# Kernel optimization log

Measured on AMD Instinct MI355X. Metric: run time of the kernel, lower is better.

The kernel has to match this reference:

```python
import jax, jax.numpy as jnp
import numpy as np

C_Z = 128
C_HIDDEN = 128
EPS = 1e-5


def _layer_norm(x, w, b):
    mu = jnp.mean(x, axis=-1, keepdims=True)
    var = jnp.var(x, axis=-1, keepdims=True)
    return (x - mu) * jax.lax.rsqrt(var + EPS) * w + b


def setup_inputs() -> dict:
    key = jax.random.key(0)
    ks = jax.random.split(key, 8)
    B, N = 1, 384
    z = jax.random.normal(ks[0], (B, N, N, C_Z), dtype=jnp.float32)
    mask = jnp.ones((B, N, N), dtype=jnp.float32)
    s_z = 1.0 / np.sqrt(C_Z)
    s_h = 1.0 / np.sqrt(C_HIDDEN)
    return {
        "z": z,
        "mask": mask,
        # projection linears (lecun-like random init)
        "w_ap": jax.random.normal(ks[1], (C_HIDDEN, C_Z), jnp.float32) * s_z,
        "b_ap": jnp.zeros((C_HIDDEN,), jnp.float32),
        "w_bp": jax.random.normal(ks[2], (C_HIDDEN, C_Z), jnp.float32) * s_z,
        "b_bp": jnp.zeros((C_HIDDEN,), jnp.float32),
        # gating linears: torch init is zeros weight / ones bias, but use small
        # random weights so gradients are non-trivial; bias = 1 as in 'gating' init
        "w_ag": jax.random.normal(ks[3], (C_HIDDEN, C_Z), jnp.float32) * s_z,
        "b_ag": jnp.ones((C_HIDDEN,), jnp.float32),
        "w_bg": jax.random.normal(ks[4], (C_HIDDEN, C_Z), jnp.float32) * s_z,
        "b_bg": jnp.ones((C_HIDDEN,), jnp.float32),
        "w_g": jax.random.normal(ks[5], (C_Z, C_Z), jnp.float32) * s_z,
        "b_g": jnp.ones((C_Z,), jnp.float32),
        # final output linear ('final' init is zeros; randomize for a useful baseline)
        "w_z": jax.random.normal(ks[6], (C_Z, C_HIDDEN), jnp.float32) * s_h,
        "b_z": jnp.zeros((C_Z,), jnp.float32),
        "ln_in_w": jnp.ones((C_Z,), jnp.float32),
        "ln_in_b": jnp.zeros((C_Z,), jnp.float32),
        "ln_out_w": jnp.ones((C_HIDDEN,), jnp.float32),
        "ln_out_b": jnp.zeros((C_HIDDEN,), jnp.float32),
    }


def reference(z, mask, w_ap, b_ap, w_bp, b_bp, w_ag, b_ag, w_bg, b_bg,
              w_g, b_g, w_z, b_z, ln_in_w, ln_in_b, ln_out_w, ln_out_b):
    # z: [B, N, N, C_z], mask: [B, N, N]
    m = mask[..., None]
    zn = _layer_norm(z, ln_in_w, ln_in_b)
    a = (zn @ w_ap.T + b_ap) * jax.nn.sigmoid(zn @ w_ag.T + b_ag) * m
    b = (zn @ w_bp.T + b_bp) * jax.nn.sigmoid(zn @ w_bg.T + b_bg) * m
    # outgoing: a -> [B,C,i,j], b -> [B,C,j,i]
    a_p = jnp.transpose(a, (0, 3, 1, 2))
    b_p = jnp.transpose(b, (0, 3, 2, 1))
    # NOTE: repo's einsum has no contracted index -> elementwise product a*b
    x = jnp.einsum('bcij,bcji->bijc', a_p, b_p)  # [B, N, N, C_hidden]
    x = _layer_norm(x, ln_out_w, ln_out_b)
    x = x @ w_z.T + b_z
    g = jax.nn.sigmoid(zn @ w_g.T + b_g)
    return x * g
```

## Files before the change

kernel.cpp:

```cpp
#include <hip/hip_runtime.h>

#define NN 384
#define CC 128
#define PP (NN*NN)
#define PB 64
#define NB (PP/PB)
#define TPB 256

typedef __attribute__((ext_vector_type(8))) short bf16x8;
typedef __attribute__((ext_vector_type(4))) float f32x4;
typedef __attribute__((ext_vector_type(8))) unsigned short u16x8;

#define PL_APH 0
#define PL_AGH 1
#define PL_BPH 2
#define PL_BGH 3
#define PL_APL 4
#define PL_AGL 5
#define PL_BPL 6
#define PL_BGL 7
#define PL_G   8
#define PL_Z   9

__device__ __forceinline__ unsigned short f2bf(float f){
  unsigned u = __float_as_uint(f);
  u += 0x7FFFu + ((u>>16)&1u);
  return (unsigned short)(u>>16);
}
__device__ __forceinline__ float bf2f(unsigned h){
  return __uint_as_float(h<<16);
}
__device__ __forceinline__ unsigned pack2(float a, float b){
  return (unsigned)f2bf(a) | ((unsigned)f2bf(b)<<16);
}
__device__ __forceinline__ float sigmoidf_(float x){
  return __fdividef(1.0f, 1.0f + __expf(-x));
}

__global__ __launch_bounds__(256) void k0_wprep(
    const float* __restrict__ wap, const float* __restrict__ wag,
    const float* __restrict__ wbp, const float* __restrict__ wbg,
    const float* __restrict__ wg,  const float* __restrict__ wz,
    unsigned short* __restrict__ wfrag){
  int tid = blockIdx.x*256 + threadIdx.x;
  int plane = tid >> 11;
  int chunk = tid & 2047;
  int mat = (plane < 8) ? (plane & 3) : (plane == 8 ? 4 : 5);
  bool lo = (plane >= 4) && (plane < 8);
  const float* W = (mat==0)?wap:(mat==1)?wag:(mat==2)?wbp:(mat==3)?wbg:(mat==4)?wg:wz;
  int k0 = chunk >> 9, n = (chunk >> 6) & 7, l = chunk & 63;
  int o  = n*16 + (l & 15);
  int kb = k0*32 + ((l>>4)<<3);
  const float* s = W + o*128 + kb;
  u16x8 v;
  #pragma unroll
  for (int e=0;e<8;e++){
    float w = s[e];
    unsigned short h = f2bf(w);
    v[e] = lo ? f2bf(w - bf2f(h)) : h;
  }
  *(u16x8*)(wfrag + (size_t)tid*8) = v;
}

__device__ __forceinline__ void stage_plane(const unsigned short* __restrict__ g,
                                            unsigned char* slot, int t){
  int wv = t>>6, l = t&63;
#if defined(__has_builtin) && __has_builtin(__builtin_amdgcn_global_load_lds)
  const unsigned char* src = (const unsigned char*)g + wv*8192 + l*16;
  unsigned char* dst = slot + wv*8192;
  #pragma unroll
  for (int i=0;i<8;i++)
    __builtin_amdgcn_global_load_lds(
        (const __attribute__((address_space(1))) unsigned int*)(src + i*1024),
        (__attribute__((address_space(3))) unsigned int*)(dst + i*1024),
        16, 0, 0);
#else
  #pragma unroll
  for (int i=0;i<8;i++)
    *(uint4*)(slot + i*4096 + t*16) =
        *(const uint4*)((const unsigned char*)g + i*4096 + t*16);
#endif
}

__device__ __forceinline__ void pass_HL(const bf16x8 aH[4], const bf16x8 aL[4],
    const unsigned char* w, int l, f32x4 acc[8]){
  #pragma unroll
  for (int k0=0;k0<4;k0++){
    #pragma unroll
    for (int n=0;n<8;n++){
      bf16x8 f = *(const bf16x8*)(w + ((k0*8+n)*64 + l)*16);
      acc[n] = __builtin_amdgcn_mfma_f32_16x16x32_bf16(aH[k0], f, acc[n], 0,0,0);
      acc[n] = __builtin_amdgcn_mfma_f32_16x16x32_bf16(aL[k0], f, acc[n], 0,0,0);
    }
  }
}

__device__ __forceinline__ void pass_H(const bf16x8 a[4],
    const unsigned char* w, int l, f32x4 acc[8]){
  #pragma unroll
  for (int k0=0;k0<4;k0++){
    #pragma unroll
    for (int n=0;n<8;n++){
      bf16x8 f = *(const bf16x8*)(w + ((k0*8+n)*64 + l)*16);
      acc[n] = __builtin_amdgcn_mfma_f32_16x16x32_bf16(a[k0], f, acc[n], 0,0,0);
    }
  }
}

__device__ __forceinline__ void bias_init(const float* __restrict__ b, int l, f32x4 acc[8]){
  #pragma unroll
  for (int n=0;n<8;n++){
    float v = b[n*16 + (l&15)];
    f32x4 iv = {v,v,v,v};
    acc[n]=iv;
  }
}

__global__ __launch_bounds__(TPB,2) void k_fused(
    const float* __restrict__ z, const float* __restrict__ mask,
    const float* __restrict__ bap, const float* __restrict__ bag,
    const float* __restrict__ bbp, const float* __restrict__ bbg,
    const float* __restrict__ bgg, const float* __restrict__ bz,
    const float* __restrict__ lniw, const float* __restrict__ lnib,
    const float* __restrict__ lnow, const float* __restrict__ lnob,
    const unsigned short* __restrict__ wfrag,
    float* __restrict__ out){
  __shared__ unsigned char lds[65536];
  unsigned char* bufH  = lds;
  unsigned char* bufL  = lds + 16384;
  unsigned char* wslot = lds + 32768;
  const int t = threadIdx.x;
  const int pos0 = blockIdx.x * PB;
  const int rowg = t>>5, c4 = (t&31)<<2;

  stage_plane(wfrag + PL_APH*16384, wslot, t);

  {
    float4 lw = *(const float4*)(lniw + c4);
    float4 lb = *(const float4*)(lnib + c4);
    #pragma unroll
    for (int it=0; it<8; ++it){
      int row = it*8 + rowg;
      float4 v = *(const float4*)(z + (size_t)(pos0+row)*CC + c4);
      float s = v.x+v.y+v.z+v.w;
      #pragma unroll
      for (int mm=1; mm<32; mm<<=1) s += __shfl_xor(s,mm);
      float mu = s*(1.0f/128.0f);
      float d0=v.x-mu, d1=v.y-mu, d2=v.z-mu, d3=v.w-mu;
      float ss = d0*d0+d1*d1+d2*d2+d3*d3;
      #pragma unroll
      for (int mm=1; mm<32; mm<<=1) ss += __shfl_xor(ss,mm);
      float rstd = rsqrtf(ss*(1.0f/128.0f) + 1e-5f);
      float n0=d0*rstd*lw.x+lb.x, n1=d1*rstd*lw.y+lb.y;
      float n2=d2*rstd*lw.z+lb.z, n3=d3*rstd*lw.w+lb.w;
      unsigned short h0=f2bf(n0), h1=f2bf(n1), h2=f2bf(n2), h3=f2bf(n3);
      unsigned off = (unsigned)(row*256 + ((c4<<1) ^ ((row&7)<<4)));
      *(uint2*)(bufH + off) = make_uint2((unsigned)h0|((unsigned)h1<<16),
                                         (unsigned)h2|((unsigned)h3<<16));
      *(uint2*)(bufL + off) = make_uint2(pack2(n0-bf2f(h0), n1-bf2f(h1)),
                                         pack2(n2-bf2f(h2), n3-bf2f(h3)));
    }
  }
  __syncthreads();

  const int wv = t>>6, l = t&63;
  const int cb = l&15;
  const int g4 = (l>>4)<<2;
  const int row0 = wv*16;

  bf16x8 aH[4], aLo[4];
  #pragma unroll
  for (int k0=0;k0<4;k0++){
    int row = row0 + cb;
    unsigned off = (unsigned)(row*256 + ((((l>>4)<<4) + (k0<<6)) ^ ((row&7)<<4)));
    aH[k0]  = *(const bf16x8*)(bufH + off);
    aLo[k0] = *(const bf16x8*)(bufL + off);
  }

  float mk[4];
  #pragma unroll
  for (int r=0;r<4;r++) mk[r] = mask[pos0 + row0 + g4 + r];

  f32x4 accp[8], accg[8];

  bias_init(bap, l, accp);
  pass_HL(aH, aLo, wslot, l, accp);
  __syncthreads();
  stage_plane(wfrag + PL_AGH*16384, wslot, t);
  __syncthreads();
  bias_init(bag, l, accg);
  pass_HL(aH, aLo, wslot, l, accg);
  __syncthreads();
  stage_plane(wfrag + PL_APL*16384, wslot, t);
  __syncthreads();
  pass_H(aH, wslot, l, accp);
  __syncthreads();
  stage_plane(wfrag + PL_AGL*16384, wslot, t);
  __syncthreads();
  pass_H(aH, wslot, l, accg);
  #pragma unroll
  for (int n=0;n<8;n++){
    #pragma unroll
    for (int r=0;r<4;r++){
      int row = row0 + g4 + r;
      int col = n*16 + cb;
      float av = accp[n][r]*sigmoidf_(accg[n][r])*mk[r];
      *(float*)(lds + row*512 + ((col<<2) ^ ((row&4)<<4))) = av;
    }
  }
  __syncthreads();
  stage_plane(wfrag + PL_BPH*16384, wslot, t);
  __syncthreads();

  bias_init(bbp, l, accp);
  pass_HL(aH, aLo, wslot, l, accp);
  __syncthreads();
  stage_plane(wfrag + PL_BGH*16384, wslot, t);
  __syncthreads();
  bias_init(bbg, l, accg);
  pass_HL(aH, aLo, wslot, l, accg);
  __syncthreads();
  stage_plane(wfrag + PL_BPL*16384, wslot, t);
  __syncthreads();
  pass_H(aH, wslot, l, accp);
  __syncthreads();
  stage_plane(wfrag + PL_BGL*16384, wslot, t);
  __syncthreads();
  pass_H(aH, wslot, l, accg);

  f32x4 xv[8];
  #pragma unroll
  for (int n=0;n<8;n++){
    #pragma unroll
    for (int r=0;r<4;r++){
      int row = row0 + g4 + r;
      int col = n*16 + cb;
      float xa = *(const float*)(lds + row*512 + ((col<<2) ^ ((row&4)<<4)));
      xv[n][r] = xa * (accp[n][r]*sigmoidf_(accg[n][r])*mk[r]);
    }
  }
  float lw8[8], lb8[8];
  #pragma unroll
  for (int n=0;n<8;n++){ lw8[n]=lnow[n*16+cb]; lb8[n]=lnob[n*16+cb]; }
  float mu_[4], rs_[4];
  #pragma unroll
  for (int r=0;r<4;r++){
    float s=0.f;
    #pragma unroll
    for (int n=0;n<8;n++) s += xv[n][r];
    #pragma unroll
    for (int mm=1; mm<16; mm<<=1) s += __shfl_xor(s,mm);
    float mu = s*(1.0f/128.0f);
    float ss=0.f;
    #pragma unroll
    for (int n=0;n<8;n++){ float d = xv[n][r]-mu; ss += d*d; }
    #pragma unroll
    for (int mm=1; mm<16; mm<<=1) ss += __shfl_xor(ss,mm);
    mu_[r] = mu;
    rs_[r] = rsqrtf(ss*(1.0f/128.0f) + 1e-5f);
  }
  __syncthreads();

  stage_plane(wfrag + PL_Z*16384, wslot, t);
  #pragma unroll
  for (int r=0;r<4;r++){
    int row = row0 + g4 + r;
    #pragma unroll
    for (int n=0;n<8;n++){
      int col = n*16 + cb;
      float v = (xv[n][r]-mu_[r])*rs_[r]*lw8[n]+lb8[n];
      *(unsigned short*)(lds + row*256 + ((col<<1) ^ ((row&7)<<4))) = f2bf(v);
    }
  }
  __syncthreads();

  bf16x8 a2[4];
  #pragma unroll
  for (int k0=0;k0<4;k0++){
    int row = row0 + cb;
    unsigned off = (unsigned)(row*256 + ((((l>>4)<<4) + (k0<<6)) ^ ((row&7)<<4)));
    a2[k0] = *(const bf16x8*)(lds + off);
  }
  f32x4 o[8], gv[8];
  bias_init(bz, l, o);
  pass_H(a2, wslot, l, o);
  __syncthreads();
  stage_plane(wfrag + PL_G*16384, wslot, t);
  __syncthreads();
  bias_init(bgg, l, gv);
  pass_H(aH, wslot, l, gv);

  #pragma unroll
  for (int r=0;r<4;r++){
    int row = row0 + g4 + r;
    #pragma unroll
    for (int n=0;n<8;n++){
      int col = n*16 + cb;
      *(float*)(lds + row*512 + ((col<<2) ^ ((row&4)<<4))) = o[n][r]*sigmoidf_(gv[n][r]);
    }
  }
  __syncthreads();
  #pragma unroll
  for (int it=0; it<8; ++it){
    int row = it*8 + rowg;
    float4 v = *(const float4*)(lds + row*512 + ((c4<<2) ^ ((row&4)<<4)));
    *(float4*)(out + (size_t)(pos0+row)*CC + c4) = v;
  }
}

extern "C" void kernel_launch(void* const* d_in, const int* in_sizes, int n_in,
                              void* d_out, int out_size, void* d_ws, size_t ws_size,
                              hipStream_t stream){
  const float* z     = (const float*)d_in[0];
  const float* mask  = (const float*)d_in[1];
  const float* w_ap  = (const float*)d_in[2];
  const float* b_ap  = (const float*)d_in[3];
  const float* w_bp  = (const float*)d_in[4];
  const float* b_bp  = (const float*)d_in[5];
  const float* w_ag  = (const float*)d_in[6];
  const float* b_ag  = (const float*)d_in[7];
  const float* w_bg  = (const float*)d_in[8];
  const float* b_bg  = (const float*)d_in[9];
  const float* w_g   = (const float*)d_in[10];
  const float* b_g   = (const float*)d_in[11];
  const float* w_z   = (const float*)d_in[12];
  const float* b_z   = (const float*)d_in[13];
  const float* ln_in_w  = (const float*)d_in[14];
  const float* ln_in_b  = (const float*)d_in[15];
  const float* ln_out_w = (const float*)d_in[16];
  const float* ln_out_b = (const float*)d_in[17];

  unsigned short* wfrag = (unsigned short*)d_ws;

  k0_wprep<<<80, 256, 0, stream>>>(w_ap, w_ag, w_bp, w_bg, w_g, w_z, wfrag);
  k_fused<<<NB, TPB, 0, stream>>>(z, mask, b_ap, b_ag, b_bp, b_bg, b_g, b_z,
                                  ln_in_w, ln_in_b, ln_out_w, ln_out_b,
                                  wfrag, (float*)d_out);
}
```

Baseline: 124.4 us.

## Switch to 32x32x16 MFMA tiles with 128-row blocks and bf16 intermediates

Doubles the rows per block to 128 and moves every GEMM from 16x16x32 to 32x32x16 bf16 MFMA, with the weight fragment layout in the prep kernel changed to match. Each block now stages the weight planes once for twice as many rows, which halves total weight staging traffic and the number of barriers per position. To fit in LDS, the lo/hi input fragments are built in turn in one region, the gated 'a' intermediate is stored as bf16 instead of fp32, and output is written straight from registers instead of through an LDS transpose. The risks are higher register pressure with 16-wide accumulators and fragment arrays, extra rounding of the 'a' value, and less coalesced output stores.

```diff
diff --git a/kernel.cpp b/kernel.cpp
--- a/kernel.cpp
+++ b/kernel.cpp
@@ -3,12 +3,12 @@
 #define NN 384
 #define CC 128
 #define PP (NN*NN)
-#define PB 64
+#define PB 128
 #define NB (PP/PB)
 #define TPB 256
 
 typedef __attribute__((ext_vector_type(8))) short bf16x8;
-typedef __attribute__((ext_vector_type(4))) float f32x4;
+typedef __attribute__((ext_vector_type(16))) float f32x16;
 typedef __attribute__((ext_vector_type(8))) unsigned short u16x8;
 
 #define PL_APH 0
@@ -21,6 +21,8 @@
 #define PL_BGL 7
 #define PL_G   8
 #define PL_Z   9
+
+#define ROWT(reg,h) ((((reg)&3) + 8*((reg)>>2)) + 4*(h))
 
 __device__ __forceinline__ unsigned short f2bf(float f){
   unsigned u = __float_as_uint(f);
@@ -48,9 +50,9 @@
   int mat = (plane < 8) ? (plane & 3) : (plane == 8 ? 4 : 5);
   bool lo = (plane >= 4) && (plane < 8);
   const float* W = (mat==0)?wap:(mat==1)?wag:(mat==2)?wbp:(mat==3)?wbg:(mat==4)?wg:wz;
-  int k0 = chunk >> 9, n = (chunk >> 6) & 7, l = chunk & 63;
-  int o  = n*16 + (l & 15);
-  int kb = k0*32 + ((l>>4)<<3);
+  int k0 = chunk >> 8, n = (chunk >> 6) & 3, l = chunk & 63;
+  int o  = n*32 + (l & 31);
+  int kb = k0*16 + ((l>>5)<<3);
   const float* s = W + o*128 + kb;
   u16x8 v;
   #pragma unroll
@@ -65,7 +67,6 @@
 __device__ __forceinline__ void stage_plane(const unsigned short* __restrict__ g,
                                             unsigned char* slot, int t){
   int wv = t>>6, l = t&63;
-#if defined(__has_builtin) && __has_builtin(__builtin_amdgcn_global_load_lds)
   const unsigned char* src = (const unsigned char*)g + wv*8192 + l*16;
   unsigned char* dst = slot + wv*8192;
   #pragma unroll
@@ -74,45 +75,52 @@
         (const __attribute__((address_space(1))) unsigned int*)(src + i*1024),
         (__attribute__((address_space(3))) unsigned int*)(dst + i*1024),
         16, 0, 0);
-#else
-  #pragma unroll
-  for (int i=0;i<8;i++)
-    *(uint4*)(slot + i*4096 + t*16) =
-        *(const uint4*)((const unsigned char*)g + i*4096 + t*16);
-#endif
-}
-
-__device__ __forceinline__ void pass_HL(const bf16x8 aH[4], const bf16x8 aL[4],
-    const unsigned char* w, int l, f32x4 acc[8]){
-  #pragma unroll
-  for (int k0=0;k0<4;k0++){
-    #pragma unroll
-    for (int n=0;n<8;n++){
-      bf16x8 f = *(const bf16x8*)(w + ((k0*8+n)*64 + l)*16);
-      acc[n] = __builtin_amdgcn_mfma_f32_16x16x32_bf16(aH[k0], f, acc[n], 0,0,0);
-      acc[n] = __builtin_amdgcn_mfma_f32_16x16x32_bf16(aL[k0], f, acc[n], 0,0,0);
-    }
-  }
-}
-
-__device__ __forceinline__ void pass_H(const bf16x8 a[4],
-    const unsigned char* w, int l, f32x4 acc[8]){
-  #pragma unroll
-  for (int k0=0;k0<4;k0++){
-    #pragma unroll
-    for (int n=0;n<8;n++){
-      bf16x8 f = *(const bf16x8*)(w + ((k0*8+n)*64 + l)*16);
-      acc[n] = __builtin_amdgcn_mfma_f32_16x16x32_bf16(a[k0], f, acc[n], 0,0,0);
-    }
-  }
-}
-
-__device__ __forceinline__ void bias_init(const float* __restrict__ b, int l, f32x4 acc[8]){
-  #pragma unroll
-  for (int n=0;n<8;n++){
-    float v = b[n*16 + (l&15)];
-    f32x4 iv = {v,v,v,v};
-    acc[n]=iv;
+}
+
+__device__ __forceinline__ void pass_HL32(const bf16x8 aH[8], const bf16x8 aL[8],
+    const unsigned char* w, int l, f32x16 acc[4]){
+  #pragma unroll
+  for (int k0=0;k0<8;k0++){
+    #pragma unroll
+    for (int n=0;n<4;n++){
+      bf16x8 f = *(const bf16x8*)(w + (k0*4+n)*1024 + l*16);
+      acc[n] = __builtin_amdgcn_mfma_f32_32x32x16_bf16(aH[k0], f, acc[n], 0,0,0);
+      acc[n] = __builtin_amdgcn_mfma_f32_32x32x16_bf16(aL[k0], f, acc[n], 0,0,0);
+    }
+  }
+}
+
+__device__ __forceinline__ void pass_H32(const bf16x8 a[8],
+    const unsigned char* w, int l, f32x16 acc[4]){
+  #pragma unroll
+  for (int k0=0;k0<8;k0++){
+    #pragma unroll
+    for (int n=0;n<4;n++){
+      bf16x8 f = *(const bf16x8*)(w + (k0*4+n)*1024 + l*16);
+      acc[n] = __builtin_amdgcn_mfma_f32_32x32x16_bf16(a[k0], f, acc[n], 0,0,0);
+    }
+  }
+}
+
+__device__ __forceinline__ void bias_init32(const float* __restrict__ b, int c,
+                                            f32x16 acc[4]){
+  #pragma unroll
+  for (int n=0;n<4;n++){
+    float v = b[n*32 + c];
+    #pragma unroll
+    for (int r=0;r<16;r++) acc[n][r] = v;
+  }
+}
+
+__device__ __forceinline__ void extract_frags(const unsigned char* base, int row0,
+                                              int l, bf16x8 a[8]){
+  int row = row0 + (l&31);
+  int hh  = (l>>5)<<4;
+  int swz = (row&7)<<4;
+  #pragma unroll
+  for (int k0=0;k0<8;k0++){
+    unsigned off = (unsigned)(row*256 + (((k0<<5) + hh) ^ swz));
+    a[k0] = *(const bf16x8*)(base + off);
   }
 }
 
@@ -126,20 +134,20 @@
     const unsigned short* __restrict__ wfrag,
     float* __restrict__ out){
   __shared__ unsigned char lds[65536];
-  unsigned char* bufH  = lds;
-  unsigned char* bufL  = lds + 16384;
-  unsigned char* wslot = lds + 32768;
+  unsigned char* R0 = lds;
+  unsigned char* R1 = lds + 32768;
   const int t = threadIdx.x;
   const int pos0 = blockIdx.x * PB;
   const int rowg = t>>5, c4 = (t&31)<<2;
 
-  stage_plane(wfrag + PL_APH*16384, wslot, t);
-
+  stage_plane(wfrag + PL_APH*16384, R1, t);
+
+  float4 nv[16];
   {
     float4 lw = *(const float4*)(lniw + c4);
     float4 lb = *(const float4*)(lnib + c4);
     #pragma unroll
-    for (int it=0; it<8; ++it){
+    for (int it=0; it<16; ++it){
       int row = it*8 + rowg;
       float4 v = *(const float4*)(z + (size_t)(pos0+row)*CC + c4);
       float s = v.x+v.y+v.z+v.w;
@@ -151,160 +159,156 @@
       #pragma unroll
       for (int mm=1; mm<32; mm<<=1) ss += __shfl_xor(ss,mm);
       float rstd = rsqrtf(ss*(1.0f/128.0f) + 1e-5f);
-      float n0=d0*rstd*lw.x+lb.x, n1=d1*rstd*lw.y+lb.y;
-      float n2=d2*rstd*lw.z+lb.z, n3=d3*rstd*lw.w+lb.w;
-      unsigned short h0=f2bf(n0), h1=f2bf(n1), h2=f2bf(n2), h3=f2bf(n3);
+      nv[it].x = d0*rstd*lw.x+lb.x; nv[it].y = d1*rstd*lw.y+lb.y;
+      nv[it].z = d2*rstd*lw.z+lb.z; nv[it].w = d3*rstd*lw.w+lb.w;
       unsigned off = (unsigned)(row*256 + ((c4<<1) ^ ((row&7)<<4)));
-      *(uint2*)(bufH + off) = make_uint2((unsigned)h0|((unsigned)h1<<16),
-                                         (unsigned)h2|((unsigned)h3<<16));
-      *(uint2*)(bufL + off) = make_uint2(pack2(n0-bf2f(h0), n1-bf2f(h1)),
-                                         pack2(n2-bf2f(h2), n3-bf2f(h3)));
+      *(uint2*)(R0 + off) = make_uint2(pack2(nv[it].x, nv[it].y),
+                                       pack2(nv[it].z, nv[it].w));
     }
   }
   __syncthreads();
 
   const int wv = t>>6, l = t&63;
-  const int cb = l&15;
-  const int g4 = (l>>4)<<2;
-  const int row0 = wv*16;
-
-  bf16x8 aH[4], aLo[4];
-  #pragma unroll
-  for (int k0=0;k0<4;k0++){
-    int row = row0 + cb;
-    unsigned off = (unsigned)(row*256 + ((((l>>4)<<4) + (k0<<6)) ^ ((row&7)<<4)));
-    aH[k0]  = *(const bf16x8*)(bufH + off);
-    aLo[k0] = *(const bf16x8*)(bufL + off);
-  }
-
-  float mk[4];
-  #pragma unroll
-  for (int r=0;r<4;r++) mk[r] = mask[pos0 + row0 + g4 + r];
-
-  f32x4 accp[8], accg[8];
-
-  bias_init(bap, l, accp);
-  pass_HL(aH, aLo, wslot, l, accp);
-  __syncthreads();
-  stage_plane(wfrag + PL_AGH*16384, wslot, t);
-  __syncthreads();
-  bias_init(bag, l, accg);
-  pass_HL(aH, aLo, wslot, l, accg);
-  __syncthreads();
-  stage_plane(wfrag + PL_APL*16384, wslot, t);
-  __syncthreads();
-  pass_H(aH, wslot, l, accp);
-  __syncthreads();
-  stage_plane(wfrag + PL_AGL*16384, wslot, t);
-  __syncthreads();
-  pass_H(aH, wslot, l, accg);
-  #pragma unroll
-  for (int n=0;n<8;n++){
-    #pragma unroll
-    for (int r=0;r<4;r++){
-      int row = row0 + g4 + r;
-      int col = n*16 + cb;
-      float av = accp[n][r]*sigmoidf_(accg[n][r])*mk[r];
-      *(float*)(lds + row*512 + ((col<<2) ^ ((row&4)<<4))) = av;
-    }
-  }
-  __syncthreads();
-  stage_plane(wfrag + PL_BPH*16384, wslot, t);
-  __syncthreads();
-
-  bias_init(bbp, l, accp);
-  pass_HL(aH, aLo, wslot, l, accp);
-  __syncthreads();
-  stage_plane(wfrag + PL_BGH*16384, wslot, t);
-  __syncthreads();
-  bias_init(bbg, l, accg);
-  pass_HL(aH, aLo, wslot, l, accg);
-  __syncthreads();
-  stage_plane(wfrag + PL_BPL*16384, wslot, t);
-  __syncthreads();
-  pass_H(aH, wslot, l, accp);
-  __syncthreads();
-  stage_plane(wfrag + PL_BGL*16384, wslot, t);
-  __syncthreads();
-  pass_H(aH, wslot, l, accg);
-
-  f32x4 xv[8];
-  #pragma unroll
-  for (int n=0;n<8;n++){
-    #pragma unroll
-    for (int r=0;r<4;r++){
-      int row = row0 + g4 + r;
-      int col = n*16 + cb;
-      float xa = *(const float*)(lds + row*512 + ((col<<2) ^ ((row&4)<<4)));
-      xv[n][r] = xa * (accp[n][r]*sigmoidf_(accg[n][r])*mk[r]);
-    }
-  }
-  float lw8[8], lb8[8];
-  #pragma unroll
-  for (int n=0;n<8;n++){ lw8[n]=lnow[n*16+cb]; lb8[n]=lnob[n*16+cb]; }
-  float mu_[4], rs_[4];
-  #pragma unroll
-  for (int r=0;r<4;r++){
-    float s=0.f;
-    #pragma unroll
-    for (int n=0;n<8;n++) s += xv[n][r];
-    #pragma unroll
-    for (int mm=1; mm<16; mm<<=1) s += __shfl_xor(s,mm);
-    float mu = s*(1.0f/128.0f);
-    float ss=0.f;
-    #pragma unroll
-    for (int n=0;n<8;n++){ float d = xv[n][r]-mu; ss += d*d; }
-    #pragma unroll
-    for (int mm=1; mm<16; mm<<=1) ss += __shfl_xor(ss,mm);
-    mu_[r] = mu;
-    rs_[r] = rsqrtf(ss*(1.0f/128.0f) + 1e-5f);
-  }
-  __syncthreads();
-
-  stage_plane(wfrag + PL_Z*16384, wslot, t);
-  #pragma unroll
-  for (int r=0;r<4;r++){
-    int row = row0 + g4 + r;
-    #pragma unroll
-    for (int n=0;n<8;n++){
-      int col = n*16 + cb;
-      float v = (xv[n][r]-mu_[r])*rs_[r]*lw8[n]+lb8[n];
-      *(unsigned short*)(lds + row*256 + ((col<<1) ^ ((row&7)<<4))) = f2bf(v);
-    }
-  }
-  __syncthreads();
-
-  bf16x8 a2[4];
-  #pragma unroll
-  for (int k0=0;k0<4;k0++){
-    int row = row0 + cb;
-    unsigned off = (unsigned)(row*256 + ((((l>>4)<<4) + (k0<<6)) ^ ((row&7)<<4)));
-    a2[k0] = *(const bf16x8*)(lds + off);
-  }
-  f32x4 o[8], gv[8];
-  bias_init(bz, l, o);
-  pass_H(a2, wslot, l, o);
-  __syncthreads();
-  stage_plane(wfrag + PL_G*16384, wslot, t);
-  __syncthreads();
-  bias_init(bgg, l, gv);
-  pass_H(aH, wslot, l, gv);
-
-  #pragma unroll
-  for (int r=0;r<4;r++){
-    int row = row0 + g4 + r;
-    #pragma unroll
-    for (int n=0;n<8;n++){
-      int col = n*16 + cb;
-      *(float*)(lds + row*512 + ((col<<2) ^ ((row&4)<<4))) = o[n][r]*sigmoidf_(gv[n][r]);
-    }
-  }
-  __syncthreads();
-  #pragma unroll
-  for (int it=0; it<8; ++it){
+  const int c  = l&31;
+  const int h  = l>>5;
+  const int row0 = wv*32;
+
+  bf16x8 aH[8], aLo[8];
+  extract_frags(R0, row0, l, aH);
+  __syncthreads();
+  #pragma unroll
+  for (int it=0; it<16; ++it){
     int row = it*8 + rowg;
-    float4 v = *(const float4*)(lds + row*512 + ((c4<<2) ^ ((row&4)<<4)));
-    *(float4*)(out + (size_t)(pos0+row)*CC + c4) = v;
+    float l0 = nv[it].x - bf2f(f2bf(nv[it].x));
+    float l1 = nv[it].y - bf2f(f2bf(nv[it].y));
+    float l2 = nv[it].z - bf2f(f2bf(nv[it].z));
+    float l3 = nv[it].w - bf2f(f2bf(nv[it].w));
+    unsigned off = (unsigned)(row*256 + ((c4<<1) ^ ((row&7)<<4)));
+    *(uint2*)(R0 + off) = make_uint2(pack2(l0,l1), pack2(l2,l3));
+  }
+  __syncthreads();
+  extract_frags(R0, row0, l, aLo);
+
+  f32x16 accp[4], accg[4];
+
+  bias_init32(bap, c, accp);
+  pass_HL32(aH, aLo, R1, l, accp);
+  __syncthreads();
+  stage_plane(wfrag + PL_AGH*16384, R1, t);
+  __syncthreads();
+  bias_init32(bag, c, accg);
+  pass_HL32(aH, aLo, R1, l, accg);
+  __syncthreads();
+  stage_plane(wfrag + PL_APL*16384, R1, t);
+  __syncthreads();
+  pass_H32(aH, R1, l, accp);
+  __syncthreads();
+  stage_plane(wfrag + PL_AGL*16384, R1, t);
+  __syncthreads();
+  pass_H32(aH, R1, l, accg);
+
+  {
+    unsigned char* xr = R0 + wv*8192;
+    #pragma unroll
+    for (int n=0;n<4;n++){
+      #pragma unroll
+      for (int j=0;j<8;j++){
+        float m0 = mask[pos0 + row0 + ROWT(2*j,   h)];
+        float m1 = mask[pos0 + row0 + ROWT(2*j+1, h)];
+        float a0 = accp[n][2*j]  *sigmoidf_(accg[n][2*j])  *m0;
+        float a1 = accp[n][2*j+1]*sigmoidf_(accg[n][2*j+1])*m1;
+        *(unsigned*)(xr + (n*8+j)*256 + l*4) = pack2(a0,a1);
+      }
+    }
+  }
+  __syncthreads();
+  stage_plane(wfrag + PL_BPH*16384, R1, t);
+  __syncthreads();
+
+  bias_init32(bbp, c, accp);
+  pass_HL32(aH, aLo, R1, l, accp);
+  __syncthreads();
+  stage_plane(wfrag + PL_BGH*16384, R1, t);
+  __syncthreads();
+  bias_init32(bbg, c, accg);
+  pass_HL32(aH, aLo, R1, l, accg);
+  __syncthreads();
+  stage_plane(wfrag + PL_BPL*16384, R1, t);
+  __syncthreads();
+  pass_H32(aH, R1, l, accp);
+  __syncthreads();
+  stage_plane(wfrag + PL_BGL*16384, R1, t);
+  __syncthreads();
+  pass_H32(aH, R1, l, accg);
+
+  f32x16 xv[4];
+  {
+    const unsigned char* xr = R0 + wv*8192;
+    #pragma unroll
+    for (int n=0;n<4;n++){
+      #pragma unroll
+      for (int j=0;j<8;j++){
+        float m0 = mask[pos0 + row0 + ROWT(2*j,   h)];
+        float m1 = mask[pos0 + row0 + ROWT(2*j+1, h)];
+        unsigned w = *(const unsigned*)(xr + (n*8+j)*256 + l*4);
+        float b0 = accp[n][2*j]  *sigmoidf_(accg[n][2*j])  *m0;
+        float b1 = accp[n][2*j+1]*sigmoidf_(accg[n][2*j+1])*m1;
+        xv[n][2*j]   = bf2f(w & 0xffffu) * b0;
+        xv[n][2*j+1] = bf2f(w >> 16)     * b1;
+      }
+    }
+  }
+  __syncthreads();
+  stage_plane(wfrag + PL_Z*16384, R1, t);
+
+  {
+    float lw4[4], lb4[4];
+    #pragma unroll
+    for (int n=0;n<4;n++){ lw4[n]=lnow[n*32+c]; lb4[n]=lnob[n*32+c]; }
+    #pragma unroll
+    for (int reg=0; reg<16; ++reg){
+      float s=0.f;
+      #pragma unroll
+      for (int n=0;n<4;n++) s += xv[n][reg];
+      #pragma unroll
+      for (int mm=1; mm<32; mm<<=1) s += __shfl_xor(s,mm);
+      float mu = s*(1.0f/128.0f);
+      float ss=0.f;
+      #pragma unroll
+      for (int n=0;n<4;n++){ float d = xv[n][reg]-mu; ss += d*d; }
+      #pragma unroll
+      for (int mm=1; mm<32; mm<<=1) ss += __shfl_xor(ss,mm);
+      float rstd = rsqrtf(ss*(1.0f/128.0f) + 1e-5f);
+      int row = row0 + ROWT(reg,h);
+      int swz = (row&7)<<4;
+      #pragma unroll
+      for (int n=0;n<4;n++){
+        int col = n*32 + c;
+        float v = (xv[n][reg]-mu)*rstd*lw4[n]+lb4[n];
+        *(unsigned short*)(R0 + row*256 + ((col<<1) ^ swz)) = f2bf(v);
+      }
+    }
+  }
+  bf16x8 a2[8];
+  extract_frags(R0, row0, l, a2);
+  __syncthreads();
+
+  f32x16 o[4], gv[4];
+  bias_init32(bz, c, o);
+  pass_H32(a2, R1, l, o);
+  __syncthreads();
+  stage_plane(wfrag + PL_G*16384, R1, t);
+  __syncthreads();
+  bias_init32(bgg, c, gv);
+  pass_H32(aH, R1, l, gv);
+
+  #pragma unroll
+  for (int n=0;n<4;n++){
+    #pragma unroll
+    for (int reg=0; reg<16; ++reg){
+      int row = row0 + ROWT(reg,h);
+      out[(size_t)(pos0+row)*CC + n*32 + c] = o[n][reg]*sigmoidf_(gv[n][reg]);
+    }
   }
 }
 
```

Measured after the change: 131.8 us. +5.9%, slower.
